# Kernel optimization log

Measured on AMD Instinct MI355X. Metric: run time of the kernel, lower is better.

## Reference

```python
import jax, jax.numpy as jnp
import numpy as np

INPUT_DIM = 256
HIDDEN_DIM = 1024
OUTPUT_DIM = 128
BATCH = 128
SEQ_LEN = 1024


def setup_inputs() -> dict:
    key = jax.random.key(0)
    ks = jax.random.split(key, 7)
    s_ih = 1.0 / np.sqrt(HIDDEN_DIM)
    return {
        "sequence": jax.random.normal(ks[0], (BATCH, SEQ_LEN, INPUT_DIM), dtype=jnp.float32),
        # nn.LSTMCell params: gates ordered (i, f, g, o), W_ih: [4H, D], W_hh: [4H, H]
        "W_ih": jax.random.uniform(ks[1], (4 * HIDDEN_DIM, INPUT_DIM), jnp.float32, -s_ih, s_ih),
        "W_hh": jax.random.uniform(ks[2], (4 * HIDDEN_DIM, HIDDEN_DIM), jnp.float32, -s_ih, s_ih),
        "b_ih": jax.random.uniform(ks[3], (4 * HIDDEN_DIM,), jnp.float32, -s_ih, s_ih),
        "b_hh": jax.random.uniform(ks[4], (4 * HIDDEN_DIM,), jnp.float32, -s_ih, s_ih),
        # nn.Linear(hidden_dim, output_dim)
        "W_out": jax.random.uniform(ks[5], (OUTPUT_DIM, HIDDEN_DIM), jnp.float32, -s_ih, s_ih),
        "b_out": jax.random.uniform(ks[6], (OUTPUT_DIM,), jnp.float32, -s_ih, s_ih),
    }


def reference(sequence, W_ih, W_hh, b_ih, b_hh, W_out, b_out):
    B = sequence.shape[0]
    H = W_hh.shape[1]
    dtype = sequence.dtype

    def step(carry, x_t):
        hx, cx = carry
        # LSTMCell: gates = x W_ih^T + b_ih + h W_hh^T + b_hh, split as (i, f, g, o)
        gates = x_t @ W_ih.T + b_ih + hx @ W_hh.T + b_hh  # [B, 4H]
        i, f, g, o = jnp.split(gates, 4, axis=-1)
        i = jax.nn.sigmoid(i)
        f = jax.nn.sigmoid(f)
        g = jnp.tanh(g)
        o = jax.nn.sigmoid(o)
        cx = f * cx + i * g
        hx = o * jnp.tanh(cx)
        # dropout p=0.0 -> identity; per-step head + log-softmax
        out = jax.nn.log_softmax(hx @ W_out.T + b_out, axis=-1)  # [B, V]
        return (hx, cx), out

    # forward loops over timesteps 0..T-2
    xs = jnp.swapaxes(sequence[:, :-1, :], 0, 1)  # [T-1, B, D]
    init = (jnp.zeros((B, H), dtype), jnp.zeros((B, H), dtype))
    _, outs = jax.lax.scan(step, init, xs)  # [T-1, B, V]
    return jnp.swapaxes(outs, 0, 1)  # [B, T-1, V]
```

## Files before the change

### kernel.cpp

```cpp
#include <hip/hip_runtime.h>

#define T_SEQ   1024
#define T_STEPS 1023
#define BATCH   128
#define DIM     256
#define HID     1024
#define VOUT    128
#define NKK     40
#define WGS     256
#define HSLOT   131072
#define SLICE_E 16384
#define XSLICE  4096

typedef __attribute__((ext_vector_type(8))) short short8;
typedef __attribute__((ext_vector_type(4))) float floatx4;

#define GLDS(gp, lp) __builtin_amdgcn_global_load_lds( \
    (const __attribute__((address_space(1))) unsigned int*)(gp), \
    (__attribute__((address_space(3))) unsigned int*)(lp), 16, 0, 0)

__device__ __forceinline__ unsigned short f2bf(float x) {
    union { float f; unsigned u; } v; v.f = x;
    unsigned r = v.u + 0x7FFFu + ((v.u >> 16) & 1u);
    return (unsigned short)(r >> 16);
}
__device__ __forceinline__ float sigm(float x) { return 1.0f / (1.0f + __expf(-x)); }


__global__ void pack_w(const float* __restrict__ Wih, const float* __restrict__ Whh,
                       unsigned short* __restrict__ Wp) {
    const size_t idx = (size_t)blockIdx.x * 256 + threadIdx.x;
    if (idx >= (size_t)32 * 8 * NKK * 64 * 8) return;
    const int j   = (int)(idx & 7);
    const int l   = (int)((idx >> 3) & 63);
    const int rest = (int)(idx >> 9);
    const int i   = rest % NKK;
    const int wcg = rest / NKK;
    const int w   = wcg & 7;
    const int cg  = wcg >> 3;
    const int cw = w >> 2, kw = w & 3;
    const int ct = i / 10, kki = i % 10;
    const int gc = cw * 64 + ct * 16 + (l & 15);
    const int R  = (gc >> 5) * HID + cg * 32 + (gc & 31);
    const int k  = (kw * 10 + kki) * 32 + (l >> 4) * 8 + j;
    const float v = (k < DIM) ? Wih[(size_t)R * DIM + k] : Whh[(size_t)R * HID + (k - DIM)];
    Wp[idx] = f2bf(v);
}

__global__ void pack_bias(const float* __restrict__ bih, const float* __restrict__ bhh,
                          float* __restrict__ bc) {
    const int idx = blockIdx.x * 256 + threadIdx.x;
    if (idx < 4096) bc[idx] = bih[idx] + bhh[idx];
}

__global__ void pack_wout(const float* __restrict__ Wo, unsigned short* __restrict__ WoBf) {
    const int idx = blockIdx.x * 256 + threadIdx.x;
    if (idx < VOUT * HID) WoBf[idx] = f2bf(Wo[idx]);
}

__global__ void pack_x(const float* __restrict__ seq, unsigned short* __restrict__ Xb) {
    const size_t idx = (size_t)blockIdx.x * 256 + threadIdx.x;
    if (idx >= (size_t)T_STEPS * BATCH * DIM) return;
    const int j   = (int)(idx & 7);
    const int row = (int)((idx >> 3) & 15);
    const int lq  = (int)((idx >> 7) & 3);
    const int kk  = (int)((idx >> 9) & 7);
    const int s8  = (int)((idx >> 12) & 7);
    const int t   = (int)(idx >> 15);
    const int b = s8 * 16 + row;
    const int k = kk * 32 + lq * 8 + j;
    Xb[idx] = f2bf(seq[((size_t)b * T_SEQ + t) * DIM + k]);
}

__global__ void init_state(unsigned short* __restrict__ Hb, int* __restrict__ bar) {
    const int idx = blockIdx.x * 256 + threadIdx.x;
    if (idx < HSLOT) Hb[idx] = 0;
    if (idx < 4096) bar[idx] = 0;
}

__global__ __launch_bounds__(512, 1) void lstm_persist(
    const unsigned short* __restrict__ Xb,
    unsigned short* __restrict__ Hblk,
    const unsigned short* __restrict__ Wp,
    const float* __restrict__ bc,
    int* __restrict__ bar)
{
    __shared__ short8 hl[2048];
    __shared__ short8 xl[512];
    __shared__ float  gl[4][16][132];
    __shared__ int abortf;

    const int wg  = blockIdx.x;
    const int s8  = wg & 7;
    const int cg  = wg >> 3;
    const int tid = threadIdx.x;
    const int w   = tid >> 6;
    const int l   = tid & 63;
    const int lr  = l & 15;
    const int lq  = l >> 4;
    const int cw  = w >> 2;
    const int kw  = w & 3;
    const int cbase = cw * 64;
    const int lq4 = lq * 4;

    const short8* wpw = (const short8*)Wp + (size_t)(cg * 8 + w) * NKK * 64 + l;
    short8 breg[NKK];
    #pragma unroll
    for (int i = 0; i < NKK; ++i) breg[i] = wpw[i * 64];

    const int er  = (tid >> 3) & 15;
    const int ej  = tid & 7;
    const int elq = tid >> 7;
    const int hc  = elq * 8 + ej;
    const float bi  = bc[0 * HID + cg * 32 + hc];
    const float bf_ = bc[1 * HID + cg * 32 + hc];
    const float bg  = bc[2 * HID + cg * 32 + hc];
    const float bo_ = bc[3 * HID + cg * 32 + hc];
    float creg = 0.f;

    if (tid == 0) abortf = 0;
    GLDS(Xb + (size_t)s8 * XSLICE + tid * 8, (unsigned short*)xl + tid * 8);

    long budget = 1L << 22;
    int* cnt = &bar[s8 * 64];
    const short8* xv = xl + l;
    const short8* hv = hl + l;

    for (int t = 0; t < T_STEPS; ++t) {
        {
            const unsigned short* hs = Hblk + (size_t)t * HSLOT + (size_t)s8 * SLICE_E;
            #pragma unroll
            for (int i = 0; i < 4; ++i)
                GLDS(hs + i * 4096 + tid * 8, (unsigned short*)hl + i * 4096 + tid * 8);
        }
        __syncthreads();

        floatx4 ac0 = {0.f,0.f,0.f,0.f}, ac1 = ac0, ac2 = ac0, ac3 = ac0;
        #define STEPK(i, av) { short8 a_ = (av); \
            ac0 = __builtin_amdgcn_mfma_f32_16x16x32_bf16(a_, breg[ 0 + (i)], ac0, 0,0,0); \
            ac1 = __builtin_amdgcn_mfma_f32_16x16x32_bf16(a_, breg[10 + (i)], ac1, 0,0,0); \
            ac2 = __builtin_amdgcn_mfma_f32_16x16x32_bf16(a_, breg[20 + (i)], ac2, 0,0,0); \
            ac3 = __builtin_amdgcn_mfma_f32_16x16x32_bf16(a_, breg[30 + (i)], ac3, 0,0,0); }
        if (kw == 0) {
            #pragma unroll
            for (int i = 0; i < 8; ++i) STEPK(i, xv[i * 64]);
            #pragma unroll
            for (int i = 8; i < 10; ++i) STEPK(i, hv[(i - 8) * 64]);
        } else {
            const short8* hb = hv + (kw * 10 - 8) * 64;
            #pragma unroll
            for (int i = 0; i < 10; ++i) STEPK(i, hb[i * 64]);
        }
        #undef STEPK

        #pragma unroll
        for (int r = 0; r < 4; ++r) {
            gl[kw][lq4 + r][cbase      + lr] = ac0[r];
            gl[kw][lq4 + r][cbase + 16 + lr] = ac1[r];
            gl[kw][lq4 + r][cbase + 32 + lr] = ac2[r];
            gl[kw][lq4 + r][cbase + 48 + lr] = ac3[r];
        }
        __syncthreads();

        float gi = bi, gf = bf_, gg = bg, go = bo_;
        #pragma unroll
        for (int q = 0; q < 4; ++q) {
            gi += gl[q][er][ 0 + hc];
            gf += gl[q][er][32 + hc];
            gg += gl[q][er][64 + hc];
            go += gl[q][er][96 + hc];
        }
        const float iv = sigm(gi), fv = sigm(gf), ov = sigm(go);
        const float gv = tanhf(gg);
        creg = fv * creg + iv * gv;
        const unsigned hu = f2bf(ov * tanhf(creg));
        const unsigned up = (unsigned)__shfl_down((int)hu, 1);
        if ((tid & 1) == 0) {
            unsigned* hp = (unsigned*)(Hblk + (size_t)(t + 1) * HSLOT
                          + (size_t)s8 * SLICE_E + (size_t)cg * 512 + tid);
            __hip_atomic_store(hp, hu | (up << 16), __ATOMIC_RELAXED, __HIP_MEMORY_SCOPE_AGENT);
        }
        __syncthreads();

        if (t + 1 < T_STEPS) {
            GLDS(Xb + (size_t)(t + 1) * (BATCH * DIM) + (size_t)s8 * XSLICE + tid * 8,
                 (unsigned short*)xl + tid * 8);
            if (tid == 0) {
                __hip_atomic_fetch_add(cnt, 1, __ATOMIC_RELAXED, __HIP_MEMORY_SCOPE_AGENT);
                while (__hip_atomic_load(cnt, __ATOMIC_RELAXED,
                                         __HIP_MEMORY_SCOPE_AGENT) < 32 * (t + 1)) {
                    __builtin_amdgcn_s_sleep(2);
                    if (--budget < 0) { abortf = 1; break; }
                }
            }
            __syncthreads();
            if (abortf) break;
        }
    }
}

__global__ __launch_bounds__(256, 2) void head_ls(
    const unsigned short* __restrict__ Hblk,
    const unsigned short* __restrict__ Wo,
    const float* __restrict__ bo,
    float* __restrict__ out)
{
    const int bg = blockIdx.x;
    const int t  = blockIdx.y;
    const int tid = threadIdx.x;
    const int w  = tid >> 6;
    const int l  = tid & 63;
    const int lr = l & 15;
    const int lq = l >> 4;
    const int b0 = bg * 16;

    const short8* ap = (const short8*)(Hblk + (size_t)(t + 1) * HSLOT
                       + (size_t)bg * SLICE_E) + l;
    const unsigned short* bp0 = Wo + (size_t)(w * 32 + lr) * HID + lq * 8;
    const unsigned short* bp1 = Wo + (size_t)(w * 32 + 16 + lr) * HID + lq * 8;

    floatx4 a0 = {0.f, 0.f, 0.f, 0.f}, a1 = {0.f, 0.f, 0.f, 0.f};
    #pragma unroll 8
    for (int kk = 0; kk < 32; ++kk) {
        short8 a   = ap[kk * 64];
        short8 b0v = *(const short8*)(bp0 + kk * 32);
        short8 b1v = *(const short8*)(bp1 + kk * 32);
        a0 = __builtin_amdgcn_mfma_f32_16x16x32_bf16(a, b0v, a0, 0, 0, 0);
        a1 = __builtin_amdgcn_mfma_f32_16x16x32_bf16(a, b1v, a1, 0, 0, 0);
    }

    __shared__ float lg[16][132];
    #pragma unroll
    for (int r = 0; r < 4; ++r) {
        lg[lq * 4 + r][w * 32 + lr]      = a0[r] + bo[w * 32 + lr];
        lg[lq * 4 + r][w * 32 + 16 + lr] = a1[r] + bo[w * 32 + 16 + lr];
    }
    __syncthreads();

    const int row = tid >> 4;
    const int c   = tid & 15;
    float vals[8];
    float m = -1e30f;
    #pragma unroll
    for (int jv = 0; jv < 8; ++jv) { vals[jv] = lg[row][c + jv * 16]; m = fmaxf(m, vals[jv]); }
    #pragma unroll
    for (int d = 8; d >= 1; d >>= 1) m = fmaxf(m, __shfl_xor(m, d, 16));
    float ssum = 0.f;
    #pragma unroll
    for (int jv = 0; jv < 8; ++jv) ssum += __expf(vals[jv] - m);
    #pragma unroll
    for (int d = 8; d >= 1; d >>= 1) ssum += __shfl_xor(ssum, d, 16);
    const float lse = m + __logf(ssum);

    float* op = out + ((size_t)(b0 + row) * T_STEPS + t) * VOUT;
    #pragma unroll
    for (int jv = 0; jv < 8; ++jv) op[c + jv * 16] = vals[jv] - lse;
}

extern "C" void kernel_launch(void* const* d_in, const int* in_sizes, int n_in,
                              void* d_out, int out_size, void* d_ws, size_t ws_size,
                              hipStream_t stream) {
    const float* seq  = (const float*)d_in[0];
    const float* Wih  = (const float*)d_in[1];
    const float* Whh  = (const float*)d_in[2];
    const float* bih  = (const float*)d_in[3];
    const float* bhh  = (const float*)d_in[4];
    const float* Wout = (const float*)d_in[5];
    const float* bout = (const float*)d_in[6];
    float* out = (float*)d_out;

    char* p = (char*)d_ws;
    unsigned short* Wp   = (unsigned short*)p; p += (size_t)32 * 8 * NKK * 64 * 8 * 2;
    unsigned short* WoBf = (unsigned short*)p; p += (size_t)VOUT * HID * 2;
    float*          bc   = (float*)p;          p += (size_t)4096 * 4;
    int*            bar  = (int*)p;            p += (size_t)4096 * 4;
    unsigned short* Xb   = (unsigned short*)p; p += (size_t)T_STEPS * BATCH * DIM * 2;
    unsigned short* Hblk = (unsigned short*)p; p += (size_t)(T_STEPS + 1) * HSLOT * 2;

    pack_w    <<<20480, 256, 0, stream>>>(Wih, Whh, Wp);
    pack_bias <<<16,    256, 0, stream>>>(bih, bhh, bc);
    pack_wout <<<512,   256, 0, stream>>>(Wout, WoBf);
    pack_x    <<<130944,256, 0, stream>>>(seq, Xb);
    init_state<<<512,   256, 0, stream>>>(Hblk, bar);

    lstm_persist<<<WGS, 512, 0, stream>>>(Xb, Hblk, Wp, bc, bar);

    head_ls<<<dim3(8, T_STEPS), 256, 0, stream>>>(Hblk, WoBf, bout, out);
}
```

Before: 3.484 ms.

## Split x/h weight paths, prefetch x-projection, use per-wave flag barrier

Splits the packed weights so only W_hh stays in registers while the W_ih slice lives in LDS. The input projection for the next step is computed before waiting on the barrier, which takes it off the serial critical path. The shared atomic counter with a single-thread spin and __syncthreads is replaced by per-workgroup flag stores that each wave polls directly, and the wave reads only the h slices it needs straight from global memory instead of staging the whole slice in LDS. The wait path loses the abort flag, so a timeout falls through silently, and the direct global reads of h rely on relaxed atomics for visibility.

```diff
diff --git a/kernel.cpp b/kernel.cpp
--- a/kernel.cpp
+++ b/kernel.cpp
@@ -6,7 +6,6 @@
 #define DIM     256
 #define HID     1024
 #define VOUT    128
-#define NKK     40
 #define WGS     256
 #define HSLOT   131072
 #define SLICE_E 16384
@@ -27,24 +26,38 @@
 __device__ __forceinline__ float sigm(float x) { return 1.0f / (1.0f + __expf(-x)); }
 
 
-__global__ void pack_w(const float* __restrict__ Wih, const float* __restrict__ Whh,
-                       unsigned short* __restrict__ Wp) {
+__global__ void pack_w(const float* __restrict__ Whh, unsigned short* __restrict__ Wph) {
     const size_t idx = (size_t)blockIdx.x * 256 + threadIdx.x;
-    if (idx >= (size_t)32 * 8 * NKK * 64 * 8) return;
+    if (idx >= (size_t)32 * 8 * 32 * 64 * 8) return;
     const int j   = (int)(idx & 7);
     const int l   = (int)((idx >> 3) & 63);
     const int rest = (int)(idx >> 9);
-    const int i   = rest % NKK;
-    const int wcg = rest / NKK;
-    const int w   = wcg & 7;
-    const int cg  = wcg >> 3;
+    const int i2  = rest & 31;
+    const int w   = (rest >> 5) & 7;
+    const int cg  = rest >> 8;
+    const int tile = i2 >> 3, hi = i2 & 7;
     const int cw = w >> 2, kw = w & 3;
-    const int ct = i / 10, kki = i % 10;
-    const int gc = cw * 64 + ct * 16 + (l & 15);
+    const int gc = cw * 64 + tile * 16 + (l & 15);
     const int R  = (gc >> 5) * HID + cg * 32 + (gc & 31);
-    const int k  = (kw * 10 + kki) * 32 + (l >> 4) * 8 + j;
-    const float v = (k < DIM) ? Wih[(size_t)R * DIM + k] : Whh[(size_t)R * HID + (k - DIM)];
-    Wp[idx] = f2bf(v);
+    const int hcol = (kw * 8 + hi) * 32 + (l >> 4) * 8 + j;
+    Wph[idx] = f2bf(Whh[(size_t)R * HID + hcol]);
+}
+
+__global__ void pack_xw(const float* __restrict__ Wih, unsigned short* __restrict__ Xw) {
+    const size_t idx = (size_t)blockIdx.x * 256 + threadIdx.x;
+    if (idx >= (size_t)32 * 8 * 8 * 64 * 8) return;
+    const int j   = (int)(idx & 7);
+    const int l   = (int)((idx >> 3) & 63);
+    const int rest = (int)(idx >> 9);
+    const int fi  = rest & 7;
+    const int w   = (rest >> 3) & 7;
+    const int cg  = rest >> 6;
+    const int tile = fi >> 1, xi = fi & 1;
+    const int cw = w >> 2, kw = w & 3;
+    const int gc = cw * 64 + tile * 16 + (l & 15);
+    const int R  = (gc >> 5) * HID + cg * 32 + (gc & 31);
+    const int xcol = (kw * 2 + xi) * 32 + (l >> 4) * 8 + j;
+    Xw[idx] = f2bf(Wih[(size_t)R * DIM + xcol]);
 }
 
 __global__ void pack_bias(const float* __restrict__ bih, const float* __restrict__ bhh,
@@ -81,14 +94,13 @@
 __global__ __launch_bounds__(512, 1) void lstm_persist(
     const unsigned short* __restrict__ Xb,
     unsigned short* __restrict__ Hblk,
-    const unsigned short* __restrict__ Wp,
+    const unsigned short* __restrict__ Wph,
+    const unsigned short* __restrict__ Xw,
     const float* __restrict__ bc,
     int* __restrict__ bar)
 {
-    __shared__ short8 hl[2048];
-    __shared__ short8 xl[512];
+    __shared__ short8 xwl[64 * 64];
     __shared__ float  gl[4][16][132];
-    __shared__ int abortf;
 
     const int wg  = blockIdx.x;
     const int s8  = wg & 7;
@@ -103,10 +115,17 @@
     const int cbase = cw * 64;
     const int lq4 = lq * 4;
 
-    const short8* wpw = (const short8*)Wp + (size_t)(cg * 8 + w) * NKK * 64 + l;
-    short8 breg[NKK];
-    #pragma unroll
-    for (int i = 0; i < NKK; ++i) breg[i] = wpw[i * 64];
+    {
+        const unsigned short* xsrc = Xw + (size_t)cg * 32768;
+        #pragma unroll
+        for (int i = 0; i < 8; ++i)
+            GLDS(xsrc + i * 4096 + tid * 8, (unsigned short*)xwl + i * 4096 + tid * 8);
+    }
+
+    const short8* wpw = (const short8*)Wph + (size_t)(cg * 8 + w) * 32 * 64 + l;
+    short8 bh[32];
+    #pragma unroll
+    for (int i = 0; i < 32; ++i) bh[i] = wpw[i * 64];
 
     const int er  = (tid >> 3) & 15;
     const int ej  = tid & 7;
@@ -118,47 +137,44 @@
     const float bo_ = bc[3 * HID + cg * 32 + hc];
     float creg = 0.f;
 
-    if (tid == 0) abortf = 0;
-    GLDS(Xb + (size_t)s8 * XSLICE + tid * 8, (unsigned short*)xl + tid * 8);
-
-    long budget = 1L << 22;
-    int* cnt = &bar[s8 * 64];
-    const short8* xv = xl + l;
-    const short8* hv = hl + l;
+    __syncthreads();
+
+    const short8* xwv = xwl + (w * 8) * 64 + l;
+    const unsigned short* hb0 = Hblk + (size_t)s8 * SLICE_E + (size_t)(kw * 8) * 512 + (size_t)l * 8;
+    const unsigned short* xa0 = Xb + (size_t)s8 * XSLICE + (size_t)(kw * 2) * 512 + (size_t)l * 8;
+    int* flagp = &bar[s8 * 64 + kw * 8 + (l & 7)];
+
+    floatx4 acx0 = {0.f,0.f,0.f,0.f}, acx1 = acx0, acx2 = acx0, acx3 = acx0;
+    #pragma unroll
+    for (int xi = 0; xi < 2; ++xi) {
+        short8 a = *(const short8*)(xa0 + xi * 512);
+        acx0 = __builtin_amdgcn_mfma_f32_16x16x32_bf16(a, xwv[(0*2+xi)*64], acx0, 0,0,0);
+        acx1 = __builtin_amdgcn_mfma_f32_16x16x32_bf16(a, xwv[(1*2+xi)*64], acx1, 0,0,0);
+        acx2 = __builtin_amdgcn_mfma_f32_16x16x32_bf16(a, xwv[(2*2+xi)*64], acx2, 0,0,0);
+        acx3 = __builtin_amdgcn_mfma_f32_16x16x32_bf16(a, xwv[(3*2+xi)*64], acx3, 0,0,0);
+    }
 
     for (int t = 0; t < T_STEPS; ++t) {
         {
-            const unsigned short* hs = Hblk + (size_t)t * HSLOT + (size_t)s8 * SLICE_E;
+            const unsigned short* hp = hb0 + (size_t)t * HSLOT;
+            short8 ha[8];
             #pragma unroll
-            for (int i = 0; i < 4; ++i)
-                GLDS(hs + i * 4096 + tid * 8, (unsigned short*)hl + i * 4096 + tid * 8);
-        }
-        __syncthreads();
-
-        floatx4 ac0 = {0.f,0.f,0.f,0.f}, ac1 = ac0, ac2 = ac0, ac3 = ac0;
-        #define STEPK(i, av) { short8 a_ = (av); \
-            ac0 = __builtin_amdgcn_mfma_f32_16x16x32_bf16(a_, breg[ 0 + (i)], ac0, 0,0,0); \
-            ac1 = __builtin_amdgcn_mfma_f32_16x16x32_bf16(a_, breg[10 + (i)], ac1, 0,0,0); \
-            ac2 = __builtin_amdgcn_mfma_f32_16x16x32_bf16(a_, breg[20 + (i)], ac2, 0,0,0); \
-            ac3 = __builtin_amdgcn_mfma_f32_16x16x32_bf16(a_, breg[30 + (i)], ac3, 0,0,0); }
-        if (kw == 0) {
+            for (int i = 0; i < 8; ++i) ha[i] = *(const short8*)(hp + i * 512);
             #pragma unroll
-            for (int i = 0; i < 8; ++i) STEPK(i, xv[i * 64]);
-            #pragma unroll
-            for (int i = 8; i < 10; ++i) STEPK(i, hv[(i - 8) * 64]);
-        } else {
-            const short8* hb = hv + (kw * 10 - 8) * 64;
-            #pragma unroll
-            for (int i = 0; i < 10; ++i) STEPK(i, hb[i * 64]);
-        }
-        #undef STEPK
+            for (int i = 0; i < 8; ++i) {
+                acx0 = __builtin_amdgcn_mfma_f32_16x16x32_bf16(ha[i], bh[ 0 + i], acx0, 0,0,0);
+                acx1 = __builtin_amdgcn_mfma_f32_16x16x32_bf16(ha[i], bh[ 8 + i], acx1, 0,0,0);
+                acx2 = __builtin_amdgcn_mfma_f32_16x16x32_bf16(ha[i], bh[16 + i], acx2, 0,0,0);
+                acx3 = __builtin_amdgcn_mfma_f32_16x16x32_bf16(ha[i], bh[24 + i], acx3, 0,0,0);
+            }
+        }
 
         #pragma unroll
         for (int r = 0; r < 4; ++r) {
-            gl[kw][lq4 + r][cbase      + lr] = ac0[r];
-            gl[kw][lq4 + r][cbase + 16 + lr] = ac1[r];
-            gl[kw][lq4 + r][cbase + 32 + lr] = ac2[r];
-            gl[kw][lq4 + r][cbase + 48 + lr] = ac3[r];
+            gl[kw][lq4 + r][cbase      + lr] = acx0[r];
+            gl[kw][lq4 + r][cbase + 16 + lr] = acx1[r];
+            gl[kw][lq4 + r][cbase + 32 + lr] = acx2[r];
+            gl[kw][lq4 + r][cbase + 48 + lr] = acx3[r];
         }
         __syncthreads();
 
@@ -183,18 +199,35 @@
         __syncthreads();
 
         if (t + 1 < T_STEPS) {
-            GLDS(Xb + (size_t)(t + 1) * (BATCH * DIM) + (size_t)s8 * XSLICE + tid * 8,
-                 (unsigned short*)xl + tid * 8);
-            if (tid == 0) {
-                __hip_atomic_fetch_add(cnt, 1, __ATOMIC_RELAXED, __HIP_MEMORY_SCOPE_AGENT);
-                while (__hip_atomic_load(cnt, __ATOMIC_RELAXED,
-                                         __HIP_MEMORY_SCOPE_AGENT) < 32 * (t + 1)) {
-                    __builtin_amdgcn_s_sleep(2);
-                    if (--budget < 0) { abortf = 1; break; }
+            if (tid == 0)
+                __hip_atomic_store(&bar[s8 * 64 + cg], t + 1,
+                                   __ATOMIC_RELAXED, __HIP_MEMORY_SCOPE_AGENT);
+
+            const unsigned short* xp = xa0 + (size_t)(t + 1) * (BATCH * DIM);
+            #pragma unroll
+            for (int xi = 0; xi < 2; ++xi) {
+                short8 a = *(const short8*)(xp + xi * 512);
+                acx0 = (xi == 0) ? __builtin_amdgcn_mfma_f32_16x16x32_bf16(a, xwv[0*64], (floatx4){0.f,0.f,0.f,0.f}, 0,0,0)
+                                 : __builtin_amdgcn_mfma_f32_16x16x32_bf16(a, xwv[1*64], acx0, 0,0,0);
+                acx1 = (xi == 0) ? __builtin_amdgcn_mfma_f32_16x16x32_bf16(a, xwv[2*64], (floatx4){0.f,0.f,0.f,0.f}, 0,0,0)
+                                 : __builtin_amdgcn_mfma_f32_16x16x32_bf16(a, xwv[3*64], acx1, 0,0,0);
+                acx2 = (xi == 0) ? __builtin_amdgcn_mfma_f32_16x16x32_bf16(a, xwv[4*64], (floatx4){0.f,0.f,0.f,0.f}, 0,0,0)
+                                 : __builtin_amdgcn_mfma_f32_16x16x32_bf16(a, xwv[5*64], acx2, 0,0,0);
+                acx3 = (xi == 0) ? __builtin_amdgcn_mfma_f32_16x16x32_bf16(a, xwv[6*64], (floatx4){0.f,0.f,0.f,0.f}, 0,0,0)
+                                 : __builtin_amdgcn_mfma_f32_16x16x32_bf16(a, xwv[7*64], acx3, 0,0,0);
+            }
+
+            {
+                const int need = t + 1;
+                int bud = 1 << 22;
+                while (true) {
+                    const int f = __hip_atomic_load(flagp, __ATOMIC_RELAXED,
+                                                    __HIP_MEMORY_SCOPE_AGENT);
+                    if (__all(f >= need)) break;
+                    if (--bud < 0) break;
                 }
+                __builtin_amdgcn_sched_barrier(0);
             }
-            __syncthreads();
-            if (abortf) break;
         }
     }
 }
@@ -270,20 +303,22 @@
     float* out = (float*)d_out;
 
     char* p = (char*)d_ws;
-    unsigned short* Wp   = (unsigned short*)p; p += (size_t)32 * 8 * NKK * 64 * 8 * 2;
+    unsigned short* Wph  = (unsigned short*)p; p += (size_t)32 * 8 * 32 * 64 * 8 * 2;
+    unsigned short* Xw   = (unsigned short*)p; p += (size_t)32 * 8 * 8 * 64 * 8 * 2;
     unsigned short* WoBf = (unsigned short*)p; p += (size_t)VOUT * HID * 2;
     float*          bc   = (float*)p;          p += (size_t)4096 * 4;
     int*            bar  = (int*)p;            p += (size_t)4096 * 4;
     unsigned short* Xb   = (unsigned short*)p; p += (size_t)T_STEPS * BATCH * DIM * 2;
     unsigned short* Hblk = (unsigned short*)p; p += (size_t)(T_STEPS + 1) * HSLOT * 2;
 
-    pack_w    <<<20480, 256, 0, stream>>>(Wih, Whh, Wp);
+    pack_w    <<<16384, 256, 0, stream>>>(Whh, Wph);
+    pack_xw   <<<4096,  256, 0, stream>>>(Wih, Xw);
     pack_bias <<<16,    256, 0, stream>>>(bih, bhh, bc);
     pack_wout <<<512,   256, 0, stream>>>(Wout, WoBf);
     pack_x    <<<130944,256, 0, stream>>>(seq, Xb);
     init_state<<<512,   256, 0, stream>>>(Hblk, bar);
 
-    lstm_persist<<<WGS, 512, 0, stream>>>(Xb, Hblk, Wp, bc, bar);
+    lstm_persist<<<WGS, 512, 0, stream>>>(Xb, Hblk, Wph, Xw, bc, bar);
 
     head_ls<<<dim3(8, T_STEPS), 256, 0, stream>>>(Hblk, WoBf, bout, out);
 }
```

After: 3.545 ms. Within noise of the previous version (+1.8%).

## Split batch into two interleaved groups with per-block flag sync and register prefetch

Applied to the files above, without the earlier changes.

Repartitions the persistent LSTM so each workgroup owns 16 hidden units for two 16-row batch groups, halving the weight registers per wave. The two batch groups are processed alternately so one group's epilogue and state publish overlap with the other group's compute and polling. The shared counter barrier is replaced by per-producer step flags, polled by lanes directly, with operands loaded straight into registers. A large dummy LDS pad is added, apparently to force one block per CU. This adds relaxed-ordering risk and complex cross-group dependencies.

```diff
diff --git a/kernel.cpp b/kernel.cpp
--- a/kernel.cpp
+++ b/kernel.cpp
@@ -6,18 +6,12 @@
 #define DIM     256
 #define HID     1024
 #define VOUT    128
-#define NKK     40
 #define WGS     256
 #define HSLOT   131072
 #define SLICE_E 16384
-#define XSLICE  4096
 
 typedef __attribute__((ext_vector_type(8))) short short8;
 typedef __attribute__((ext_vector_type(4))) float floatx4;
-
-#define GLDS(gp, lp) __builtin_amdgcn_global_load_lds( \
-    (const __attribute__((address_space(1))) unsigned int*)(gp), \
-    (__attribute__((address_space(3))) unsigned int*)(lp), 16, 0, 0)
 
 __device__ __forceinline__ unsigned short f2bf(float x) {
     union { float f; unsigned u; } v; v.f = x;
@@ -30,20 +24,21 @@
 __global__ void pack_w(const float* __restrict__ Wih, const float* __restrict__ Whh,
                        unsigned short* __restrict__ Wp) {
     const size_t idx = (size_t)blockIdx.x * 256 + threadIdx.x;
-    if (idx >= (size_t)32 * 8 * NKK * 64 * 8) return;
+    if (idx >= (size_t)64 * 8 * 2 * 10 * 64 * 8) return;
     const int j   = (int)(idx & 7);
     const int l   = (int)((idx >> 3) & 63);
     const int rest = (int)(idx >> 9);
-    const int i   = rest % NKK;
-    const int wcg = rest / NKK;
-    const int w   = wcg & 7;
-    const int cg  = wcg >> 3;
+    const int kki  = rest % 10;
+    const int rest2 = rest / 10;
+    const int ct  = rest2 & 1;
+    const int w   = (rest2 >> 1) & 7;
+    const int cg  = rest2 >> 4;
     const int cw = w >> 2, kw = w & 3;
-    const int ct = i / 10, kki = i % 10;
-    const int gc = cw * 64 + ct * 16 + (l & 15);
-    const int R  = (gc >> 5) * HID + cg * 32 + (gc & 31);
-    const int k  = (kw * 10 + kki) * 32 + (l >> 4) * 8 + j;
-    const float v = (k < DIM) ? Wih[(size_t)R * DIM + k] : Whh[(size_t)R * HID + (k - DIM)];
+    const int lgc = cw * 32 + ct * 16 + (l & 15);
+    const int gate = lgc >> 4, p = lgc & 15;
+    const int R = gate * HID + cg * 16 + p;
+    const int k = kw * 320 + kki * 32 + (l >> 4) * 8 + j;
+    const float v = (k < 256) ? Wih[(size_t)R * DIM + k] : Whh[(size_t)R * HID + (k - 256)];
     Wp[idx] = f2bf(v);
 }
 
@@ -64,11 +59,12 @@
     const int j   = (int)(idx & 7);
     const int row = (int)((idx >> 3) & 15);
     const int lq  = (int)((idx >> 7) & 3);
-    const int kk  = (int)((idx >> 9) & 7);
-    const int s8  = (int)((idx >> 12) & 7);
+    const int xk  = (int)((idx >> 9) & 7);
+    const int sp  = (int)((idx >> 12) & 3);
+    const int ga  = (int)((idx >> 14) & 1);
     const int t   = (int)(idx >> 15);
-    const int b = s8 * 16 + row;
-    const int k = kk * 32 + lq * 8 + j;
+    const int b = ga * 64 + sp * 16 + row;
+    const int k = xk * 32 + lq * 8 + j;
     Xb[idx] = f2bf(seq[((size_t)b * T_SEQ + t) * DIM + k]);
 }
 
@@ -85,118 +81,137 @@
     const float* __restrict__ bc,
     int* __restrict__ bar)
 {
-    __shared__ short8 hl[2048];
-    __shared__ short8 xl[512];
-    __shared__ float  gl[4][16][132];
-    __shared__ int abortf;
+    __shared__ float gl[2][4][16][68];
+    __shared__ unsigned short hstage[2][256];
+    __shared__ char icepad[61440];
 
     const int wg  = blockIdx.x;
-    const int s8  = wg & 7;
-    const int cg  = wg >> 3;
+    const int sp  = wg & 3;
+    const int cg  = wg >> 2;
     const int tid = threadIdx.x;
     const int w   = tid >> 6;
     const int l   = tid & 63;
     const int lr  = l & 15;
     const int lq  = l >> 4;
+    const int kw  = w & 3;
     const int cw  = w >> 2;
-    const int kw  = w & 3;
-    const int cbase = cw * 64;
+    const int cwb = cw * 32;
     const int lq4 = lq * 4;
-
-    const short8* wpw = (const short8*)Wp + (size_t)(cg * 8 + w) * NKK * 64 + l;
-    short8 breg[NKK];
-    #pragma unroll
-    for (int i = 0; i < NKK; ++i) breg[i] = wpw[i * 64];
-
-    const int er  = (tid >> 3) & 15;
-    const int ej  = tid & 7;
-    const int elq = tid >> 7;
-    const int hc  = elq * 8 + ej;
-    const float bi  = bc[0 * HID + cg * 32 + hc];
-    const float bf_ = bc[1 * HID + cg * 32 + hc];
-    const float bg  = bc[2 * HID + cg * 32 + hc];
-    const float bo_ = bc[3 * HID + cg * 32 + hc];
-    float creg = 0.f;
-
-    if (tid == 0) abortf = 0;
-    GLDS(Xb + (size_t)s8 * XSLICE + tid * 8, (unsigned short*)xl + tid * 8);
-
-    long budget = 1L << 22;
-    int* cnt = &bar[s8 * 64];
-    const short8* xv = xl + l;
-    const short8* hv = hl + l;
+    const int gsA = sp;
+    const int gsB = 4 + sp;
+
+    if (tid == 511 && bar[4000] != 0) icepad[bar[4001] & 32767] = 1;
+
+    const short8* wpw = (const short8*)Wp + (size_t)((cg * 8 + w) * 20) * 64 + l;
+    short8 bw[20];
+    #pragma unroll
+    for (int i = 0; i < 20; ++i) bw[i] = wpw[i * 64];
+
+    const int er = (tid >> 4) & 15;
+    const int ep = tid & 15;
+    const int hsi = ((ep >> 3) * 16 + er) * 8 + (ep & 7);
+    const float bi  = bc[0 * HID + cg * 16 + ep];
+    const float bf_ = bc[1 * HID + cg * 16 + ep];
+    const float bg  = bc[2 * HID + cg * 16 + ep];
+    const float bo_ = bc[3 * HID + cg * 16 + ep];
+    float cregA = 0.f, cregB = 0.f;
+
+    const int cnt  = (kw == 0) ? 4 : 20;
+    const int base = (kw == 0) ? 0 : (kw * 20 - 16);
+    const int pcg  = base + (l % cnt);
+    const unsigned short* xbA = Xb + (size_t)gsA * 4096;
+    const unsigned short* xbB = Xb + (size_t)gsB * 4096;
+
+    const floatx4 zf4 = {0.f, 0.f, 0.f, 0.f};
+    short8 avA[10], avB[10];
+
+#define POLL_PREF(AV, GS, XBASE, NN) { \
+    const int* fp_ = bar + (GS) * 64 + pcg; \
+    int budl_ = 1 << 20; \
+    while (true) { \
+        const int f_ = __hip_atomic_load(fp_, __ATOMIC_RELAXED, __HIP_MEMORY_SCOPE_AGENT); \
+        if (__all(f_ >= (NN))) break; \
+        if (--budl_ < 0) break; \
+    } \
+    __builtin_amdgcn_sched_barrier(0); \
+    if (kw == 0) { \
+        const unsigned short* xp_ = (XBASE) + (size_t)(NN) * 32768 + (size_t)l * 8; \
+        _Pragma("unroll") \
+        for (int i_ = 0; i_ < 8; ++i_) AV[i_] = *(const short8*)(xp_ + i_ * 512); \
+        const unsigned short* hp_ = Hblk + (size_t)(NN) * HSLOT + (size_t)(GS) * SLICE_E + (size_t)l * 8; \
+        AV[8] = *(const short8*)(hp_); \
+        AV[9] = *(const short8*)(hp_ + 512); \
+    } else { \
+        const unsigned short* hp_ = Hblk + (size_t)(NN) * HSLOT + (size_t)(GS) * SLICE_E \
+            + (size_t)(kw * 10 - 8) * 512 + (size_t)l * 8; \
+        _Pragma("unroll") \
+        for (int i_ = 0; i_ < 10; ++i_) AV[i_] = *(const short8*)(hp_ + i_ * 512); \
+    } }
+
+#define COMPUTE_GL(G, AV) { \
+    floatx4 a0_ = zf4, a1_ = zf4; \
+    _Pragma("unroll") \
+    for (int i_ = 0; i_ < 10; ++i_) { \
+        a0_ = __builtin_amdgcn_mfma_f32_16x16x32_bf16(AV[i_], bw[i_],      a0_, 0, 0, 0); \
+        a1_ = __builtin_amdgcn_mfma_f32_16x16x32_bf16(AV[i_], bw[10 + i_], a1_, 0, 0, 0); \
+    } \
+    _Pragma("unroll") \
+    for (int rr_ = 0; rr_ < 4; ++rr_) { \
+        gl[G][kw][lq4 + rr_][cwb + lr]      = a0_[rr_]; \
+        gl[G][kw][lq4 + rr_][cwb + 16 + lr] = a1_[rr_]; \
+    } }
+
+#define EPI_STAGE(G, CREG) { \
+    __syncthreads(); \
+    if (tid < 256) { \
+        float gi_ = bi, gf_ = bf_, gg_ = bg, go_ = bo_; \
+        _Pragma("unroll") \
+        for (int q_ = 0; q_ < 4; ++q_) { \
+            gi_ += gl[G][q_][er][ 0 + ep]; \
+            gf_ += gl[G][q_][er][16 + ep]; \
+            gg_ += gl[G][q_][er][32 + ep]; \
+            go_ += gl[G][q_][er][48 + ep]; \
+        } \
+        const float iv_ = sigm(gi_), fv_ = sigm(gf_), ov_ = sigm(go_); \
+        const float gv_ = tanhf(gg_); \
+        CREG = fv_ * CREG + iv_ * gv_; \
+        hstage[G][hsi] = f2bf(ov_ * tanhf(CREG)); \
+    } \
+    __syncthreads(); }
+
+#define W7_STORE_FLAG(G, GS, TS) { \
+    if (w == 7) { \
+        const unsigned* hu_ = (const unsigned*)&hstage[G][l * 4]; \
+        const unsigned u0_ = hu_[0], u1_ = hu_[1]; \
+        const unsigned long long vv_ = u0_ | ((unsigned long long)u1_ << 32); \
+        unsigned long long* hp_ = (unsigned long long*)(Hblk \
+            + (size_t)(TS) * HSLOT + (size_t)(GS) * SLICE_E \
+            + (size_t)(cg >> 1) * 512 + (size_t)(cg & 1) * 256) + l; \
+        __hip_atomic_store(hp_, vv_, __ATOMIC_RELAXED, __HIP_MEMORY_SCOPE_AGENT); \
+        asm volatile("s_waitcnt vmcnt(0)" ::: "memory"); \
+        if (l == 0) \
+            __hip_atomic_store(bar + (GS) * 64 + cg, (TS), \
+                               __ATOMIC_RELAXED, __HIP_MEMORY_SCOPE_AGENT); \
+    } }
+
+    POLL_PREF(avA, gsA, xbA, 0);
 
     for (int t = 0; t < T_STEPS; ++t) {
-        {
-            const unsigned short* hs = Hblk + (size_t)t * HSLOT + (size_t)s8 * SLICE_E;
-            #pragma unroll
-            for (int i = 0; i < 4; ++i)
-                GLDS(hs + i * 4096 + tid * 8, (unsigned short*)hl + i * 4096 + tid * 8);
-        }
-        __syncthreads();
-
-        floatx4 ac0 = {0.f,0.f,0.f,0.f}, ac1 = ac0, ac2 = ac0, ac3 = ac0;
-        #define STEPK(i, av) { short8 a_ = (av); \
-            ac0 = __builtin_amdgcn_mfma_f32_16x16x32_bf16(a_, breg[ 0 + (i)], ac0, 0,0,0); \
-            ac1 = __builtin_amdgcn_mfma_f32_16x16x32_bf16(a_, breg[10 + (i)], ac1, 0,0,0); \
-            ac2 = __builtin_amdgcn_mfma_f32_16x16x32_bf16(a_, breg[20 + (i)], ac2, 0,0,0); \
-            ac3 = __builtin_amdgcn_mfma_f32_16x16x32_bf16(a_, breg[30 + (i)], ac3, 0,0,0); }
-        if (kw == 0) {
-            #pragma unroll
-            for (int i = 0; i < 8; ++i) STEPK(i, xv[i * 64]);
-            #pragma unroll
-            for (int i = 8; i < 10; ++i) STEPK(i, hv[(i - 8) * 64]);
-        } else {
-            const short8* hb = hv + (kw * 10 - 8) * 64;
-            #pragma unroll
-            for (int i = 0; i < 10; ++i) STEPK(i, hb[i * 64]);
-        }
-        #undef STEPK
-
-        #pragma unroll
-        for (int r = 0; r < 4; ++r) {
-            gl[kw][lq4 + r][cbase      + lr] = ac0[r];
-            gl[kw][lq4 + r][cbase + 16 + lr] = ac1[r];
-            gl[kw][lq4 + r][cbase + 32 + lr] = ac2[r];
-            gl[kw][lq4 + r][cbase + 48 + lr] = ac3[r];
-        }
-        __syncthreads();
-
-        float gi = bi, gf = bf_, gg = bg, go = bo_;
-        #pragma unroll
-        for (int q = 0; q < 4; ++q) {
-            gi += gl[q][er][ 0 + hc];
-            gf += gl[q][er][32 + hc];
-            gg += gl[q][er][64 + hc];
-            go += gl[q][er][96 + hc];
-        }
-        const float iv = sigm(gi), fv = sigm(gf), ov = sigm(go);
-        const float gv = tanhf(gg);
-        creg = fv * creg + iv * gv;
-        const unsigned hu = f2bf(ov * tanhf(creg));
-        const unsigned up = (unsigned)__shfl_down((int)hu, 1);
-        if ((tid & 1) == 0) {
-            unsigned* hp = (unsigned*)(Hblk + (size_t)(t + 1) * HSLOT
-                          + (size_t)s8 * SLICE_E + (size_t)cg * 512 + tid);
-            __hip_atomic_store(hp, hu | (up << 16), __ATOMIC_RELAXED, __HIP_MEMORY_SCOPE_AGENT);
-        }
-        __syncthreads();
-
-        if (t + 1 < T_STEPS) {
-            GLDS(Xb + (size_t)(t + 1) * (BATCH * DIM) + (size_t)s8 * XSLICE + tid * 8,
-                 (unsigned short*)xl + tid * 8);
-            if (tid == 0) {
-                __hip_atomic_fetch_add(cnt, 1, __ATOMIC_RELAXED, __HIP_MEMORY_SCOPE_AGENT);
-                while (__hip_atomic_load(cnt, __ATOMIC_RELAXED,
-                                         __HIP_MEMORY_SCOPE_AGENT) < 32 * (t + 1)) {
-                    __builtin_amdgcn_s_sleep(2);
-                    if (--budget < 0) { abortf = 1; break; }
-                }
-            }
-            __syncthreads();
-            if (abortf) break;
-        }
+        POLL_PREF(avB, gsB, xbB, t);
+
+        COMPUTE_GL(0, avA);
+        EPI_STAGE(0, cregA);
+        W7_STORE_FLAG(0, gsA, t + 1);
+
+        COMPUTE_GL(1, avB);
+        EPI_STAGE(1, cregB);
+        if (t + 1 < T_STEPS) POLL_PREF(avA, gsA, xbA, t + 1);
+        W7_STORE_FLAG(1, gsB, t + 1);
     }
+#undef POLL_PREF
+#undef COMPUTE_GL
+#undef EPI_STAGE
+#undef W7_STORE_FLAG
 }
 
 __global__ __launch_bounds__(256, 2) void head_ls(
@@ -270,7 +285,7 @@
     float* out = (float*)d_out;
 
     char* p = (char*)d_ws;
-    unsigned short* Wp   = (unsigned short*)p; p += (size_t)32 * 8 * NKK * 64 * 8 * 2;
+    unsigned short* Wp   = (unsigned short*)p; p += (size_t)64 * 8 * 2 * 10 * 64 * 8 * 2;
     unsigned short* WoBf = (unsigned short*)p; p += (size_t)VOUT * HID * 2;
     float*          bc   = (float*)p;          p += (size_t)4096 * 4;
     int*            bar  = (int*)p;            p += (size_t)4096 * 4;
```

Measured after the change: 11.35 ms. 3.26x slower.
